# Performance work log

Measured on AMD Instinct MI355X. Metric: run time of the kernel, lower is better.

Reference implementation:

```python
import jax, jax.numpy as jnp
import numpy as np

D_IN = 1024
D_OUT = 1024
NUM_HEADS = 16
HEAD_DIM = D_OUT // NUM_HEADS


def setup_inputs() -> dict:
    key = jax.random.key(0)
    k_x, k_q, k_k, k_v, k_o = jax.random.split(key, 5)
    # Xavier-uniform-ish init for weights (stored as [d_in, d_out] for x @ W)
    lim = float(np.sqrt(6.0 / (D_IN + D_OUT)) / np.sqrt(2.0))
    lim_o = float(np.sqrt(6.0 / (D_OUT + D_OUT)))
    return {
        "x": jax.random.normal(k_x, (2, 2048, D_IN), dtype=jnp.float32),
        "W_query": jax.random.uniform(k_q, (D_IN, D_OUT), jnp.float32, -lim, lim),
        "W_key": jax.random.uniform(k_k, (D_IN, D_OUT), jnp.float32, -lim, lim),
        "W_value": jax.random.uniform(k_v, (D_IN, D_OUT), jnp.float32, -lim, lim),
        "W_out": jax.random.uniform(k_o, (D_OUT, D_OUT), jnp.float32, -lim_o, lim_o),
        "b_out": jnp.zeros((D_OUT,), dtype=jnp.float32),
    }


def reference(x, W_query, W_key, W_value, W_out, b_out):
    B, S, _ = x.shape
    scale = 1.0 / np.sqrt(HEAD_DIM)

    def split_heads(t):  # [B,S,D] -> [B,H,S,hd]
        return t.reshape(B, S, NUM_HEADS, HEAD_DIM).transpose(0, 2, 1, 3)

    q = split_heads(x @ W_query)
    k = split_heads(x @ W_key)
    v = split_heads(x @ W_value)

    scores = jnp.einsum("bhqd,bhkd->bhqk", q, k) * scale  # [B,H,S,S]
    causal = jnp.tril(jnp.ones((S, S), dtype=bool))  # True = keep
    scores = jnp.where(causal, scores, -jnp.inf)
    weights = jax.nn.softmax(scores, axis=-1)
    ctx = jnp.einsum("bhqk,bhkd->bhqd", weights, v)
    ctx = ctx.transpose(0, 2, 1, 3).reshape(B, S, D_OUT)
    return ctx @ W_out + b_out
```

## Files before the change

### kernel.cpp

```cpp
#include <hip/hip_runtime.h>
#include <hip/hip_bf16.h>


typedef __bf16 bf16_t;
typedef __bf16 bf16x4 __attribute__((ext_vector_type(4)));
typedef __bf16 bf16x8 __attribute__((ext_vector_type(8)));
typedef float f32x4 __attribute__((ext_vector_type(4)));

#define AS_GLOBAL __attribute__((address_space(1)))
#define AS_LDS    __attribute__((address_space(3)))

__device__ __forceinline__ void async_load16(const void* g, void* l) {
    __builtin_amdgcn_global_load_lds((AS_GLOBAL void*)(g), (AS_LDS void*)(l), 16, 0, 0);
}

__global__ __launch_bounds__(256) void cvt_f32_bf16(const float* __restrict__ src,
                                                    bf16_t* __restrict__ dst, int n4) {
    int i = blockIdx.x * 256 + threadIdx.x;
    if (i < n4) {
        float4 v = ((const float4*)src)[i];
        bf16x4 o;
        o[0] = (bf16_t)v.x; o[1] = (bf16_t)v.y; o[2] = (bf16_t)v.z; o[3] = (bf16_t)v.w;
        ((bf16x4*)dst)[i] = o;
    }
}

__global__ __launch_bounds__(256) void transpose_cvt4(
    const float* __restrict__ W0, const float* __restrict__ W1,
    const float* __restrict__ W2, const float* __restrict__ W3,
    bf16_t* __restrict__ outbase) {
    __shared__ bf16_t T[64][65];
    int t = threadIdx.x;
    int k0 = blockIdx.x * 64, n0 = blockIdx.y * 64, z = blockIdx.z;
    const float* W = (z == 0) ? W0 : (z == 1) ? W1 : (z == 2) ? W2 : W3;
    bf16_t* WT = outbase + (size_t)z * 1048576;
#pragma unroll
    for (int c = 0; c < 4; c++) {
        int idx = c * 256 + t;
        int row = idx >> 4;
        int col4 = (idx & 15) * 4;
        float4 v = *(const float4*)(W + (k0 + row) * 1024 + n0 + col4);
        T[row][col4 + 0] = (bf16_t)v.x;
        T[row][col4 + 1] = (bf16_t)v.y;
        T[row][col4 + 2] = (bf16_t)v.z;
        T[row][col4 + 3] = (bf16_t)v.w;
    }
    __syncthreads();
#pragma unroll
    for (int c = 0; c < 4; c++) {
        int idx = c * 256 + t;
        int nrow = idx >> 4;
        int kc4 = (idx & 15) * 4;
        bf16x4 o;
        o[0] = T[kc4 + 0][nrow];
        o[1] = T[kc4 + 1][nrow];
        o[2] = T[kc4 + 2][nrow];
        o[3] = T[kc4 + 3][nrow];
        *(bf16x4*)(WT + (n0 + nrow) * 1024 + k0 + kc4) = o;
    }
}

__global__ __launch_bounds__(256) void qkv_gemm(
    const bf16_t* __restrict__ A,
    const bf16_t* __restrict__ WqT, const bf16_t* __restrict__ WkT,
    const bf16_t* __restrict__ WvT,
    bf16_t* __restrict__ Qo, bf16_t* __restrict__ Ko, bf16_t* __restrict__ Vo) {
    const int KD = 1024;
    __shared__ bf16_t As[2][128 * 32];
    __shared__ bf16_t Bs[2][128 * 32];
    int tid = threadIdx.x;
    int wave = tid >> 6, lane = tid & 63;
    int quad = lane >> 4, l16 = lane & 15;
    int wm = wave >> 1, wn = wave & 1;
    int z = blockIdx.z;
    const bf16_t* BT = (z == 0) ? WqT : (z == 1) ? WkT : WvT;
    int m0 = blockIdx.x * 128;
    int n0 = blockIdx.y * 128;

    int r = tid >> 2;
    int c8 = (((tid & 3) ^ ((tid >> 3) & 3))) * 8;
    const bf16_t* gA0 = A + (size_t)(m0 + r) * KD + c8;
    const bf16_t* gA1 = A + (size_t)(m0 + 64 + r) * KD + c8;
    const bf16_t* gB0 = BT + (size_t)(n0 + r) * KD + c8;
    const bf16_t* gB1 = BT + (size_t)(n0 + 64 + r) * KD + c8;

    f32x4 acc[4][4];
#pragma unroll
    for (int i = 0; i < 4; i++)
#pragma unroll
        for (int j = 0; j < 4; j++) acc[i][j] = (f32x4){0.f, 0.f, 0.f, 0.f};

    async_load16(gA0, As[0] + wave * 512);
    async_load16(gA1, As[0] + 2048 + wave * 512);
    async_load16(gB0, Bs[0] + wave * 512);
    async_load16(gB1, Bs[0] + 2048 + wave * 512);
    __syncthreads();

    for (int kk = 0; kk < 32; kk++) {
        int cur = kk & 1;
        if (kk < 31) {
            int k0 = (kk + 1) * 32;
            async_load16(gA0 + k0, As[cur ^ 1] + wave * 512);
            async_load16(gA1 + k0, As[cur ^ 1] + 2048 + wave * 512);
            async_load16(gB0 + k0, Bs[cur ^ 1] + wave * 512);
            async_load16(gB1 + k0, Bs[cur ^ 1] + 2048 + wave * 512);
        }
        bf16x8 af[4], bfr[4];
        int csw = (quad ^ ((l16 >> 1) & 3)) * 8;
#pragma unroll
        for (int mt = 0; mt < 4; mt++)
            af[mt] = *(const bf16x8*)(As[cur] + (wm * 64 + mt * 16 + l16) * 32 + csw);
#pragma unroll
        for (int nt = 0; nt < 4; nt++)
            bfr[nt] = *(const bf16x8*)(Bs[cur] + (wn * 64 + nt * 16 + l16) * 32 + csw);
        if (z == 2) {
#pragma unroll
            for (int mt = 0; mt < 4; mt++)
#pragma unroll
                for (int nt = 0; nt < 4; nt++)
                    acc[mt][nt] = __builtin_amdgcn_mfma_f32_16x16x32_bf16(
                        bfr[nt], af[mt], acc[mt][nt], 0, 0, 0);
        } else {
#pragma unroll
            for (int mt = 0; mt < 4; mt++)
#pragma unroll
                for (int nt = 0; nt < 4; nt++)
                    acc[mt][nt] = __builtin_amdgcn_mfma_f32_16x16x32_bf16(
                        af[mt], bfr[nt], acc[mt][nt], 0, 0, 0);
        }
        __syncthreads();
    }

    if (z == 0) {
#pragma unroll
        for (int mt = 0; mt < 4; mt++) {
            int mg_base = m0 + wm * 64 + mt * 16 + quad * 4;
#pragma unroll
            for (int nt = 0; nt < 4; nt++) {
                int ng = n0 + wn * 64 + nt * 16 + l16;
                int h = ng >> 6, d = ng & 63;
#pragma unroll
                for (int rr = 0; rr < 4; rr++) {
                    int mg = mg_base + rr;
                    int b = mg >> 11, s = mg & 2047;
                    Qo[(((size_t)(b * 16 + h) * 2048) + s) * 64 + d] =
                        (bf16_t)acc[mt][nt][rr];
                }
            }
        }
    } else if (z == 1) {
#pragma unroll
        for (int mt = 0; mt < 4; mt++) {
            int mg_base = m0 + wm * 64 + mt * 16 + quad * 4;
#pragma unroll
            for (int nt = 0; nt < 4; nt++) {
                int ng = n0 + wn * 64 + nt * 16 + l16;
                int h = ng >> 6, dd = ng & 63;
#pragma unroll
                for (int rr = 0; rr < 4; rr++) {
                    int mg = mg_base + rr;
                    int b = mg >> 11, sl = mg & 2047;
                    int kt = sl >> 6, row = sl & 63;
                    int cc = (dd >> 3) ^ (row & 7);
                    Ko[(size_t)(b * 16 + h) * 131072 + kt * 4096 + row * 64 +
                       cc * 8 + (dd & 7)] = (bf16_t)acc[mt][nt][rr];
                }
            }
        }
    } else {
#pragma unroll
        for (int mt = 0; mt < 4; mt++) {
            int sg = m0 + wm * 64 + mt * 16 + l16;
            int b = sg >> 11, sl = sg & 2047;
            int kt = sl >> 6, srow = sl & 63;
#pragma unroll
            for (int nt = 0; nt < 4; nt++) {
                int dg_base = n0 + wn * 64 + nt * 16 + quad * 4;
#pragma unroll
                for (int rr = 0; rr < 4; rr++) {
                    int dg = dg_base + rr;
                    int h = dg >> 6, dd = dg & 63;
                    int cc = (srow >> 3) ^ (dd & 7);
                    Vo[(size_t)(b * 16 + h) * 131072 + kt * 4096 + dd * 64 +
                       cc * 8 + (srow & 7)] = (bf16_t)acc[mt][nt][rr];
                }
            }
        }
    }
}

__device__ __forceinline__ float exp_pwrite(f32x4 sc[4], bf16_t* Ps,
                                            int wave, int quad, int l16) {
    float part = 0.f;
    int rowbase = (wave * 16 + l16) * 64;
    int gran = (quad & 1) * 4;
    int chi = quad >> 1;
#pragma unroll
    for (int nt = 0; nt < 4; nt++) {
        f32x4 p;
#pragma unroll
        for (int rr = 0; rr < 4; rr++) {
            p[rr] = __builtin_amdgcn_exp2f(sc[nt][rr]);
            part += p[rr];
        }
        bf16x4 pb;
#pragma unroll
        for (int rr = 0; rr < 4; rr++) pb[rr] = (bf16_t)p[rr];
        int cc = (nt * 2 + chi) ^ (l16 & 7);
        *(bf16x4*)(Ps + rowbase + cc * 8 + gran) = pb;
    }
    part += __shfl_xor(part, 16);
    part += __shfl_xor(part, 32);
    return part;
}

__global__ __launch_bounds__(256) void attn(
    const bf16_t* __restrict__ Q, const bf16_t* __restrict__ Kt,
    const bf16_t* __restrict__ Vt, bf16_t* __restrict__ ctx) {
    const int S = 2048;
    __shared__ bf16_t Ks[2][4096];
    __shared__ bf16_t Vs[2][4096];
    __shared__ bf16_t Ps[4096];
    int tid = threadIdx.x, wave = tid >> 6, lane = tid & 63;
    int quad = lane >> 4, l16 = lane & 15;

    int f = blockIdx.x + 32 * blockIdx.y;
    int g = f >> 8, s = f & 255;
    int qt = (g & 1) ? (31 - (s & 31)) : (s & 31);
    int bh = (s >> 5) + 8 * g;
    int h = bh & 15, b = bh >> 4;

    const bf16_t* Qbh = Q + (size_t)bh * S * 64;
    const bf16_t* Kbh = Kt + (size_t)bh * 131072;
    const bf16_t* Vbh = Vt + (size_t)bh * 131072;

    const float qs = 0.125f * 1.44269504f;
    bf16x8 aQ[2];
    {
        const bf16_t* rq = Qbh + (size_t)(qt * 64 + wave * 16 + l16) * 64;
#pragma unroll
        for (int ks = 0; ks < 2; ks++) {
            bf16x8 t = *(const bf16x8*)(rq + ks * 32 + quad * 8);
#pragma unroll
            for (int j = 0; j < 8; j++) t[j] = (bf16_t)((float)t[j] * qs);
            aQ[ks] = t;
        }
    }

    float L = 0.f;
    f32x4 O[4];
#pragma unroll
    for (int i = 0; i < 4; i++) O[i] = (f32x4){0.f, 0.f, 0.f, 0.f};

    {
        const bf16_t* kg = Kbh + tid * 8;
        const bf16_t* vg = Vbh + tid * 8;
        async_load16(kg, Ks[0] + wave * 512);
        async_load16(kg + 2048, Ks[0] + 2048 + wave * 512);
        async_load16(vg, Vs[0] + wave * 512);
        async_load16(vg + 2048, Vs[0] + 2048 + wave * 512);
    }
    __syncthreads();

    for (int kt = 0; kt <= qt; kt++) {
        int cur = kt & 1;
        if (kt < qt) {
            const bf16_t* kg = Kbh + (kt + 1) * 4096 + tid * 8;
            const bf16_t* vg = Vbh + (kt + 1) * 4096 + tid * 8;
            async_load16(kg, Ks[cur ^ 1] + wave * 512);
            async_load16(kg + 2048, Ks[cur ^ 1] + 2048 + wave * 512);
            async_load16(vg, Vs[cur ^ 1] + wave * 512);
            async_load16(vg + 2048, Vs[cur ^ 1] + 2048 + wave * 512);
        }

        bf16x8 kf[4][2], vf[4][2];
#pragma unroll
        for (int nt = 0; nt < 4; nt++) {
            const bf16_t* krow = Ks[cur] + (nt * 16 + l16) * 64;
            const bf16_t* vrow = Vs[cur] + (nt * 16 + l16) * 64;
#pragma unroll
            for (int ks = 0; ks < 2; ks++) {
                int csw = ((ks * 4 + quad) ^ (l16 & 7)) * 8;
                kf[nt][ks] = *(const bf16x8*)(krow + csw);
                vf[nt][ks] = *(const bf16x8*)(vrow + csw);
            }
        }

        f32x4 sc[4];
#pragma unroll
        for (int nt = 0; nt < 4; nt++) {
            f32x4 ss = (f32x4){0.f, 0.f, 0.f, 0.f};
            ss = __builtin_amdgcn_mfma_f32_16x16x32_bf16(kf[nt][0], aQ[0], ss, 0, 0, 0);
            ss = __builtin_amdgcn_mfma_f32_16x16x32_bf16(kf[nt][1], aQ[1], ss, 0, 0, 0);
            sc[nt] = ss;
        }
        if (kt == qt) {
            int qg = qt * 64 + wave * 16 + l16;
#pragma unroll
            for (int nt = 0; nt < 4; nt++)
#pragma unroll
                for (int rr = 0; rr < 4; rr++)
                    if (kt * 64 + nt * 16 + quad * 4 + rr > qg) sc[nt][rr] = -1e30f;
        }
        L += exp_pwrite(sc, Ps, wave, quad, l16);

#pragma unroll
        for (int ks = 0; ks < 2; ks++) {
            int csw = ((ks * 4 + quad) ^ (l16 & 7)) * 8;
            bf16x8 aP = *(const bf16x8*)(Ps + (wave * 16 + l16) * 64 + csw);
#pragma unroll
            for (int nt = 0; nt < 4; nt++)
                O[nt] = __builtin_amdgcn_mfma_f32_16x16x32_bf16(aP, vf[nt][ks],
                                                                O[nt], 0, 0, 0);
        }
        __syncthreads();
    }

    float il[4];
#pragma unroll
    for (int rr = 0; rr < 4; rr++) il[rr] = 1.f / __shfl(L, quad * 4 + rr);
#pragma unroll
    for (int nt = 0; nt < 4; nt++) {
#pragma unroll
        for (int rr = 0; rr < 4; rr++) {
            int qoff = wave * 16 + quad * 4 + rr;
            int col = h * 64 + nt * 16 + l16;
            ctx[(size_t)(b * 2048 + qt * 64 + qoff) * 1024 + col] =
                (bf16_t)(O[nt][rr] * il[rr]);
        }
    }
}

__global__ __launch_bounds__(256) void out_gemm(
    const bf16_t* __restrict__ A, const bf16_t* __restrict__ BT,
    const float* __restrict__ bias, float* __restrict__ Cout) {
    const int KD = 1024;
    __shared__ bf16_t As[2][64 * 32];
    __shared__ bf16_t Bs[2][128 * 32];
    int tid = threadIdx.x;
    int wave = tid >> 6, lane = tid & 63;
    int quad = lane >> 4, l16 = lane & 15;
    int wm = wave >> 1, wn = wave & 1;
    int m0 = blockIdx.x * 64;
    int n0 = blockIdx.y * 128;

    int r = tid >> 2;
    int c8 = (((tid & 3) ^ ((tid >> 3) & 3))) * 8;
    const bf16_t* gA  = A + (size_t)(m0 + r) * KD + c8;
    const bf16_t* gB0 = BT + (size_t)(n0 + r) * KD + c8;
    const bf16_t* gB1 = BT + (size_t)(n0 + 64 + r) * KD + c8;

    f32x4 acc[2][4];
#pragma unroll
    for (int i = 0; i < 2; i++)
#pragma unroll
        for (int j = 0; j < 4; j++) acc[i][j] = (f32x4){0.f, 0.f, 0.f, 0.f};

    async_load16(gA, As[0] + wave * 512);
    async_load16(gB0, Bs[0] + wave * 512);
    async_load16(gB1, Bs[0] + 2048 + wave * 512);
    __syncthreads();

    for (int kk = 0; kk < 32; kk++) {
        int cur = kk & 1;
        if (kk < 31) {
            int k0 = (kk + 1) * 32;
            async_load16(gA + k0, As[cur ^ 1] + wave * 512);
            async_load16(gB0 + k0, Bs[cur ^ 1] + wave * 512);
            async_load16(gB1 + k0, Bs[cur ^ 1] + 2048 + wave * 512);
        }
        bf16x8 af[2], bfr[4];
        int csw = (quad ^ ((l16 >> 1) & 3)) * 8;
#pragma unroll
        for (int mt = 0; mt < 2; mt++)
            af[mt] = *(const bf16x8*)(As[cur] + (wm * 32 + mt * 16 + l16) * 32 + csw);
#pragma unroll
        for (int nt = 0; nt < 4; nt++)
            bfr[nt] = *(const bf16x8*)(Bs[cur] + (wn * 64 + nt * 16 + l16) * 32 + csw);
#pragma unroll
        for (int mt = 0; mt < 2; mt++)
#pragma unroll
            for (int nt = 0; nt < 4; nt++)
                acc[mt][nt] = __builtin_amdgcn_mfma_f32_16x16x32_bf16(af[mt], bfr[nt],
                                                                      acc[mt][nt], 0, 0, 0);
        __syncthreads();
    }

#pragma unroll
    for (int mt = 0; mt < 2; mt++) {
        int mg_base = m0 + wm * 32 + mt * 16 + quad * 4;
#pragma unroll
        for (int nt = 0; nt < 4; nt++) {
            int ng = n0 + wn * 64 + nt * 16 + l16;
            float bv = bias[ng];
#pragma unroll
            for (int rr = 0; rr < 4; rr++) {
                int mg = mg_base + rr;
                Cout[(size_t)mg * 1024 + ng] = acc[mt][nt][rr] + bv;
            }
        }
    }
}

extern "C" void kernel_launch(void* const* d_in, const int* in_sizes, int n_in,
                              void* d_out, int out_size, void* d_ws, size_t ws_size,
                              hipStream_t stream) {
    const float* x  = (const float*)d_in[0];
    const float* Wq = (const float*)d_in[1];
    const float* Wk = (const float*)d_in[2];
    const float* Wv = (const float*)d_in[3];
    const float* Wo = (const float*)d_in[4];
    const float* bo = (const float*)d_in[5];
    float* out = (float*)d_out;
    char* ws = (char*)d_ws;

    bf16_t* xb   = (bf16_t*)(ws);
    bf16_t* WTs  = (bf16_t*)(ws + (8u << 20));
    bf16_t* WqT  = WTs;
    bf16_t* WkT  = WTs + 1048576;
    bf16_t* WvT  = WTs + 2097152;
    bf16_t* WoT  = WTs + 3145728;
    bf16_t* Qb   = (bf16_t*)(ws + (16u << 20));
    bf16_t* Kb   = (bf16_t*)(ws + (24u << 20));
    bf16_t* Vb   = (bf16_t*)(ws + (32u << 20));
    bf16_t* ctxb = (bf16_t*)(ws + (40u << 20));

    cvt_f32_bf16<<<4096, 256, 0, stream>>>(x, xb, (4096 * 1024) / 4);
    transpose_cvt4<<<dim3(16, 16, 4), 256, 0, stream>>>(Wq, Wk, Wv, Wo, WTs);
    qkv_gemm<<<dim3(32, 8, 3), 256, 0, stream>>>(xb, WqT, WkT, WvT, Qb, Kb, Vb);
    attn<<<dim3(32, 32), 256, 0, stream>>>(Qb, Kb, Vb, ctxb);
    out_gemm<<<dim3(64, 8), 256, 0, stream>>>(ctxb, WoT, bo, out);
}
```

Measured before the change: 218.2 us.

## Replace async global-to-LDS loads with register-staged prefetch in both GEMMs

The QKV and output-projection GEMMs no longer use global_load_lds async copies followed by a full __syncthreads each k-step. Each thread now prefetches the next k-tile into registers, writes it into the alternate LDS buffer after reading the current fragments, and uses a custom lgkmcnt-wait-plus-barrier, with the loop manually unrolled by two. The aim is to hide global load latency behind MFMA work and cut barrier and vmcnt wait overhead. The cost is extra VGPRs for the staging registers and reliance on the hand-written barrier to order the LDS writes and reads correctly.

Result: faster. 186.6 us (-14.5%).

```diff
diff --git a/kernel.cpp b/kernel.cpp
--- a/kernel.cpp
+++ b/kernel.cpp
@@ -12,6 +12,10 @@
 
 __device__ __forceinline__ void async_load16(const void* g, void* l) {
     __builtin_amdgcn_global_load_lds((AS_GLOBAL void*)(g), (AS_LDS void*)(l), 16, 0, 0);
+}
+
+__device__ __forceinline__ void barrier_lgkm() {
+    asm volatile("s_waitcnt lgkmcnt(0)\n\ts_barrier" ::: "memory");
 }
 
 __global__ __launch_bounds__(256) void cvt_f32_bf16(const float* __restrict__ src,
@@ -66,8 +70,8 @@
     const bf16_t* __restrict__ WvT,
     bf16_t* __restrict__ Qo, bf16_t* __restrict__ Ko, bf16_t* __restrict__ Vo) {
     const int KD = 1024;
-    __shared__ bf16_t As[2][128 * 32];
-    __shared__ bf16_t Bs[2][128 * 32];
+    __shared__ __align__(16) bf16_t As[2][4096];
+    __shared__ __align__(16) bf16_t Bs[2][4096];
     int tid = threadIdx.x;
     int wave = tid >> 6, lane = tid & 63;
     int quad = lane >> 4, l16 = lane & 15;
@@ -90,29 +94,35 @@
 #pragma unroll
         for (int j = 0; j < 4; j++) acc[i][j] = (f32x4){0.f, 0.f, 0.f, 0.f};
 
-    async_load16(gA0, As[0] + wave * 512);
-    async_load16(gA1, As[0] + 2048 + wave * 512);
-    async_load16(gB0, Bs[0] + wave * 512);
-    async_load16(gB1, Bs[0] + 2048 + wave * 512);
-    __syncthreads();
-
-    for (int kk = 0; kk < 32; kk++) {
-        int cur = kk & 1;
-        if (kk < 31) {
-            int k0 = (kk + 1) * 32;
-            async_load16(gA0 + k0, As[cur ^ 1] + wave * 512);
-            async_load16(gA1 + k0, As[cur ^ 1] + 2048 + wave * 512);
-            async_load16(gB0 + k0, Bs[cur ^ 1] + wave * 512);
-            async_load16(gB1 + k0, Bs[cur ^ 1] + 2048 + wave * 512);
-        }
+    int4 sa0 = *(const int4*)gA0, sa1 = *(const int4*)gA1;
+    int4 sb0 = *(const int4*)gB0, sb1 = *(const int4*)gB1;
+    *(int4*)(As[0] + tid * 8) = sa0;
+    *(int4*)(As[0] + 2048 + tid * 8) = sa1;
+    *(int4*)(Bs[0] + tid * 8) = sb0;
+    *(int4*)(Bs[0] + 2048 + tid * 8) = sb1;
+    sa0 = *(const int4*)(gA0 + 32); sa1 = *(const int4*)(gA1 + 32);
+    sb0 = *(const int4*)(gB0 + 32); sb1 = *(const int4*)(gB1 + 32);
+
+    int csw = (quad ^ ((l16 >> 1) & 3)) * 8;
+#pragma unroll 1
+    for (int kk = 0; kk < 32; kk += 2) {
+        barrier_lgkm();
         bf16x8 af[4], bfr[4];
-        int csw = (quad ^ ((l16 >> 1) & 3)) * 8;
 #pragma unroll
         for (int mt = 0; mt < 4; mt++)
-            af[mt] = *(const bf16x8*)(As[cur] + (wm * 64 + mt * 16 + l16) * 32 + csw);
+            af[mt] = *(const bf16x8*)(As[0] + (wm * 64 + mt * 16 + l16) * 32 + csw);
 #pragma unroll
         for (int nt = 0; nt < 4; nt++)
-            bfr[nt] = *(const bf16x8*)(Bs[cur] + (wn * 64 + nt * 16 + l16) * 32 + csw);
+            bfr[nt] = *(const bf16x8*)(Bs[0] + (wn * 64 + nt * 16 + l16) * 32 + csw);
+        *(int4*)(As[1] + tid * 8) = sa0;
+        *(int4*)(As[1] + 2048 + tid * 8) = sa1;
+        *(int4*)(Bs[1] + tid * 8) = sb0;
+        *(int4*)(Bs[1] + 2048 + tid * 8) = sb1;
+        if (kk + 2 < 32) {
+            int k0 = (kk + 2) * 32;
+            sa0 = *(const int4*)(gA0 + k0); sa1 = *(const int4*)(gA1 + k0);
+            sb0 = *(const int4*)(gB0 + k0); sb1 = *(const int4*)(gB1 + k0);
+        }
         if (z == 2) {
 #pragma unroll
             for (int mt = 0; mt < 4; mt++)
@@ -128,7 +138,39 @@
                     acc[mt][nt] = __builtin_amdgcn_mfma_f32_16x16x32_bf16(
                         af[mt], bfr[nt], acc[mt][nt], 0, 0, 0);
         }
-        __syncthreads();
+        barrier_lgkm();
+#pragma unroll
+        for (int mt = 0; mt < 4; mt++)
+            af[mt] = *(const bf16x8*)(As[1] + (wm * 64 + mt * 16 + l16) * 32 + csw);
+#pragma unroll
+        for (int nt = 0; nt < 4; nt++)
+            bfr[nt] = *(const bf16x8*)(Bs[1] + (wn * 64 + nt * 16 + l16) * 32 + csw);
+        if (kk + 2 < 32) {
+            *(int4*)(As[0] + tid * 8) = sa0;
+            *(int4*)(As[0] + 2048 + tid * 8) = sa1;
+            *(int4*)(Bs[0] + tid * 8) = sb0;
+            *(int4*)(Bs[0] + 2048 + tid * 8) = sb1;
+            if (kk + 3 < 32) {
+                int k0 = (kk + 3) * 32;
+                sa0 = *(const int4*)(gA0 + k0); sa1 = *(const int4*)(gA1 + k0);
+                sb0 = *(const int4*)(gB0 + k0); sb1 = *(const int4*)(gB1 + k0);
+            }
+        }
+        if (z == 2) {
+#pragma unroll
+            for (int mt = 0; mt < 4; mt++)
+#pragma unroll
+                for (int nt = 0; nt < 4; nt++)
+                    acc[mt][nt] = __builtin_amdgcn_mfma_f32_16x16x32_bf16(
+                        bfr[nt], af[mt], acc[mt][nt], 0, 0, 0);
+        } else {
+#pragma unroll
+            for (int mt = 0; mt < 4; mt++)
+#pragma unroll
+                for (int nt = 0; nt < 4; nt++)
+                    acc[mt][nt] = __builtin_amdgcn_mfma_f32_16x16x32_bf16(
+                        af[mt], bfr[nt], acc[mt][nt], 0, 0, 0);
+        }
     }
 
     if (z == 0) {
@@ -335,8 +377,8 @@
     const bf16_t* __restrict__ A, const bf16_t* __restrict__ BT,
     const float* __restrict__ bias, float* __restrict__ Cout) {
     const int KD = 1024;
-    __shared__ bf16_t As[2][64 * 32];
-    __shared__ bf16_t Bs[2][128 * 32];
+    __shared__ __align__(16) bf16_t As[2][2048];
+    __shared__ __align__(16) bf16_t Bs[2][4096];
     int tid = threadIdx.x;
     int wave = tid >> 6, lane = tid & 63;
     int quad = lane >> 4, l16 = lane & 15;
@@ -356,34 +398,62 @@
 #pragma unroll
         for (int j = 0; j < 4; j++) acc[i][j] = (f32x4){0.f, 0.f, 0.f, 0.f};
 
-    async_load16(gA, As[0] + wave * 512);
-    async_load16(gB0, Bs[0] + wave * 512);
-    async_load16(gB1, Bs[0] + 2048 + wave * 512);
-    __syncthreads();
-
-    for (int kk = 0; kk < 32; kk++) {
-        int cur = kk & 1;
-        if (kk < 31) {
-            int k0 = (kk + 1) * 32;
-            async_load16(gA + k0, As[cur ^ 1] + wave * 512);
-            async_load16(gB0 + k0, Bs[cur ^ 1] + wave * 512);
-            async_load16(gB1 + k0, Bs[cur ^ 1] + 2048 + wave * 512);
-        }
+    int4 sa = *(const int4*)gA;
+    int4 sb0 = *(const int4*)gB0, sb1 = *(const int4*)gB1;
+    *(int4*)(As[0] + tid * 8) = sa;
+    *(int4*)(Bs[0] + tid * 8) = sb0;
+    *(int4*)(Bs[0] + 2048 + tid * 8) = sb1;
+    sa = *(const int4*)(gA + 32);
+    sb0 = *(const int4*)(gB0 + 32); sb1 = *(const int4*)(gB1 + 32);
+
+    int csw = (quad ^ ((l16 >> 1) & 3)) * 8;
+#pragma unroll 1
+    for (int kk = 0; kk < 32; kk += 2) {
+        barrier_lgkm();
         bf16x8 af[2], bfr[4];
-        int csw = (quad ^ ((l16 >> 1) & 3)) * 8;
 #pragma unroll
         for (int mt = 0; mt < 2; mt++)
-            af[mt] = *(const bf16x8*)(As[cur] + (wm * 32 + mt * 16 + l16) * 32 + csw);
+            af[mt] = *(const bf16x8*)(As[0] + (wm * 32 + mt * 16 + l16) * 32 + csw);
 #pragma unroll
         for (int nt = 0; nt < 4; nt++)
-            bfr[nt] = *(const bf16x8*)(Bs[cur] + (wn * 64 + nt * 16 + l16) * 32 + csw);
+            bfr[nt] = *(const bf16x8*)(Bs[0] + (wn * 64 + nt * 16 + l16) * 32 + csw);
+        *(int4*)(As[1] + tid * 8) = sa;
+        *(int4*)(Bs[1] + tid * 8) = sb0;
+        *(int4*)(Bs[1] + 2048 + tid * 8) = sb1;
+        if (kk + 2 < 32) {
+            int k0 = (kk + 2) * 32;
+            sa = *(const int4*)(gA + k0);
+            sb0 = *(const int4*)(gB0 + k0); sb1 = *(const int4*)(gB1 + k0);
+        }
 #pragma unroll
         for (int mt = 0; mt < 2; mt++)
 #pragma unroll
             for (int nt = 0; nt < 4; nt++)
                 acc[mt][nt] = __builtin_amdgcn_mfma_f32_16x16x32_bf16(af[mt], bfr[nt],
                                                                       acc[mt][nt], 0, 0, 0);
-        __syncthreads();
+        barrier_lgkm();
+#pragma unroll
+        for (int mt = 0; mt < 2; mt++)
+            af[mt] = *(const bf16x8*)(As[1] + (wm * 32 + mt * 16 + l16) * 32 + csw);
+#pragma unroll
+        for (int nt = 0; nt < 4; nt++)
+            bfr[nt] = *(const bf16x8*)(Bs[1] + (wn * 64 + nt * 16 + l16) * 32 + csw);
+        if (kk + 2 < 32) {
+            *(int4*)(As[0] + tid * 8) = sa;
+            *(int4*)(Bs[0] + tid * 8) = sb0;
+            *(int4*)(Bs[0] + 2048 + tid * 8) = sb1;
+            if (kk + 3 < 32) {
+                int k0 = (kk + 3) * 32;
+                sa = *(const int4*)(gA + k0);
+                sb0 = *(const int4*)(gB0 + k0); sb1 = *(const int4*)(gB1 + k0);
+            }
+        }
+#pragma unroll
+        for (int mt = 0; mt < 2; mt++)
+#pragma unroll
+            for (int nt = 0; nt < 4; nt++)
+                acc[mt][nt] = __builtin_amdgcn_mfma_f32_16x16x32_bf16(af[mt], bfr[nt],
+                                                                      acc[mt][nt], 0, 0, 0);
     }
 
 #pragma unroll
```
